# Performance work log

Measured on AMD Instinct MI355X. Metric: run time of the kernel, lower is better.

## Reference

```python
import jax, jax.numpy as jnp
import numpy as np

D_MODEL, D_BLOOM, N_HEADS = 768, 64, 4
HEAD_DIM = D_MODEL // N_HEADS


def setup_inputs() -> dict:
    key = jax.random.key(0)
    ks = jax.random.split(key, 16)
    B, S = 8, 1024
    s = 0.02
    return {
        "dnabert_hidden": jax.random.normal(ks[0], (B, S, D_MODEL), jnp.float32),
        "bloom_encoding": jax.random.uniform(ks[1], (B, S, D_BLOOM), jnp.float32),
        "Wq": jax.random.normal(ks[2], (D_MODEL, D_MODEL), jnp.float32) * s,
        "bq": jnp.zeros((D_MODEL,), jnp.float32),
        "Wk": jax.random.normal(ks[3], (D_BLOOM, D_MODEL), jnp.float32) * s,
        "bk": jnp.zeros((D_MODEL,), jnp.float32),
        "Wv": jax.random.normal(ks[4], (D_MODEL, D_MODEL), jnp.float32) * s,
        "bv": jnp.zeros((D_MODEL,), jnp.float32),
        "Wb1": jax.random.normal(ks[5], (D_BLOOM, N_HEADS * 2), jnp.float32) * s,
        "bb1": jnp.zeros((N_HEADS * 2,), jnp.float32),
        "Wb2": jax.random.normal(ks[6], (N_HEADS * 2, N_HEADS), jnp.float32) * s,
        "bb2": jnp.zeros((N_HEADS,), jnp.float32),
        "Wo": jax.random.normal(ks[7], (D_MODEL, D_MODEL), jnp.float32) * s,
        "bo": jnp.zeros((D_MODEL,), jnp.float32),
        "ln_g": jnp.ones((D_MODEL,), jnp.float32),
        "ln_b": jnp.zeros((D_MODEL,), jnp.float32),
    }


def reference(dnabert_hidden, bloom_encoding, Wq, bq, Wk, bk, Wv, bv,
              Wb1, bb1, Wb2, bb2, Wo, bo, ln_g, ln_b):
    B, S, _ = dnabert_hidden.shape
    H, Dh = N_HEADS, HEAD_DIM
    # projections -> [B, H, S, Dh]
    Q = (dnabert_hidden @ Wq + bq).reshape(B, S, H, Dh).transpose(0, 2, 1, 3)
    K = (bloom_encoding @ Wk + bk).reshape(B, S, H, Dh).transpose(0, 2, 1, 3)
    V = (dnabert_hidden @ Wv + bv).reshape(B, S, H, Dh).transpose(0, 2, 1, 3)
    scores = jnp.einsum('bhqd,bhkd->bhqk', Q, K) / jnp.sqrt(jnp.float32(Dh))
    # bloom bias MLP: [B, S, H] -> broadcast over query positions as [B, H, 1, S]
    h = jax.nn.gelu(bloom_encoding @ Wb1 + bb1, approximate=False)
    bias = (h @ Wb2 + bb2).transpose(0, 2, 1)[:, :, None, :]
    attn = jax.nn.softmax(scores + bias, axis=-1)  # dropout is identity in eval
    ctx = jnp.einsum('bhqk,bhkd->bhqd', attn, V)
    ctx = ctx.transpose(0, 2, 1, 3).reshape(B, S, H * Dh)
    out = ctx @ Wo + bo
    x = out + dnabert_hidden
    mu = jnp.mean(x, axis=-1, keepdims=True)
    var = jnp.var(x, axis=-1, keepdims=True)
    y = (x - mu) * jax.lax.rsqrt(var + 1e-5) * ln_g + ln_b
    return y, attn
```

## Files before the change

kernel.cpp:

```cpp
#include <hip/hip_runtime.h>
#include <hip/hip_bf16.h>
#include <math.h>
#include <stdint.h>

typedef __bf16 bf16;
typedef __bf16 bf16x8 __attribute__((ext_vector_type(8)));
typedef __bf16 bf16x4v __attribute__((ext_vector_type(4)));
typedef float f32x4 __attribute__((ext_vector_type(4)));

#define NHEADS 4
#define DM 768
#define DB 64
#define HD 192
#define BATCH 8
#define SEQ 1024
#define MROWS 8192
#define SCALE 0.07216878364870323f

__device__ __forceinline__ void gld_lds16(const void* g, void* l) {
  __builtin_amdgcn_global_load_lds(
      (__attribute__((address_space(1))) void*)(void*)g,
      (__attribute__((address_space(3))) void*)l, 16, 0, 0);
}

__global__ __launch_bounds__(256) void prologue(
    const float* __restrict__ Xd, bf16* __restrict__ Xd_bf,
    const float* __restrict__ Xb, bf16* __restrict__ Xb_bf,
    const float* __restrict__ Wq, const float* __restrict__ Wv,
    const float* __restrict__ Wk, const float* __restrict__ Wo,
    bf16* __restrict__ WT0, bf16* __restrict__ WT1,
    bf16* __restrict__ WT2, bf16* __restrict__ WT3,
    const float* __restrict__ Wb1, const float* __restrict__ bb1,
    const float* __restrict__ Wb2, const float* __restrict__ bb2,
    float* __restrict__ biasarr) {
  __shared__ float Lt[64 * 65];
  const int id = blockIdx.x;
  const int tid = threadIdx.x;
  if (id < 6656) {
    const float* in = (id < 6144) ? Xd : Xb;
    bf16* out = (id < 6144) ? Xd_bf : Xb_bf;
    long i = (long)(id < 6144 ? id : id - 6144) * 256 + tid;
    f32x4 v = *(const f32x4*)&in[i * 4];
    bf16x4v t;
    t[0] = (bf16)v[0]; t[1] = (bf16)v[1]; t[2] = (bf16)v[2]; t[3] = (bf16)v[3];
    *(bf16x4v*)&out[i * 4] = t;
  } else if (id < 6688) {
    int idx = (id - 6656) * 256 + tid;
    const float* x = Xb + (long)idx * DB;
    float h[8];
#pragma unroll
    for (int j = 0; j < 8; ++j) h[j] = bb1[j];
    for (int k = 0; k < DB; ++k) {
      float xv = x[k];
#pragma unroll
      for (int j = 0; j < 8; ++j) h[j] = fmaf(xv, Wb1[k * 8 + j], h[j]);
    }
#pragma unroll
    for (int j = 0; j < 8; ++j) {
      float a = h[j];
      h[j] = 0.5f * a * (1.0f + erff(a * 0.7071067811865476f));
    }
    int b = idx >> 10, s = idx & 1023;
#pragma unroll
    for (int o = 0; o < 4; ++o) {
      float a = bb2[o];
#pragma unroll
      for (int j = 0; j < 8; ++j) a = fmaf(h[j], Wb2[j * 4 + o], a);
      biasarr[((long)(b * 4 + o) << 10) + s] = a;
    }
  } else {
    int wi = id - 6688;
    const float* W;
    bf16* WT;
    int K, tIdx;
    if (wi < 144)      { W = Wq; WT = WT0; K = DM; tIdx = wi; }
    else if (wi < 288) { W = Wv; WT = WT1; K = DM; tIdx = wi - 144; }
    else if (wi < 300) { W = Wk; WT = WT2; K = DB; tIdx = wi - 288; }
    else               { W = Wo; WT = WT3; K = DM; tIdx = wi - 300; }
    const int tk0 = (tIdx / 12) * 64;
    const int tn0 = (tIdx % 12) * 64;
#pragma unroll
    for (int p = 0; p < 4; ++p) {
      int r = p * 16 + (tid >> 4);
      int c = (tid & 15) * 4;
      f32x4 v = *(const f32x4*)&W[(long)(tk0 + r) * DM + tn0 + c];
      Lt[r * 65 + c] = v[0]; Lt[r * 65 + c + 1] = v[1];
      Lt[r * 65 + c + 2] = v[2]; Lt[r * 65 + c + 3] = v[3];
    }
    __syncthreads();
    const int n = tid >> 2, kg = (tid & 3) * 16;
    bf16x8 o0, o1;
#pragma unroll
    for (int e = 0; e < 8; ++e) {
      o0[e] = (bf16)Lt[(kg + e) * 65 + n];
      o1[e] = (bf16)Lt[(kg + 8 + e) * 65 + n];
    }
    *(bf16x8*)&WT[(long)(tn0 + n) * K + tk0 + kg] = o0;
    *(bf16x8*)&WT[(long)(tn0 + n) * K + tk0 + kg + 8] = o1;
  }
}

__global__ __launch_bounds__(256) void rowsum_scale_f32(float* __restrict__ attn) {
  const int row = blockIdx.x * 4 + (threadIdx.x >> 6);
  const int lane = threadIdx.x & 63;
  float* ar = attn + ((long)row << 10);
  f32x4 v[4];
#pragma unroll
  for (int i = 0; i < 4; ++i) v[i] = *(const f32x4*)&ar[i * 256 + lane * 4];
  float s = 0.0f;
#pragma unroll
  for (int i = 0; i < 4; ++i)
#pragma unroll
    for (int j = 0; j < 4; ++j) s += v[i][j];
  for (int d = 1; d < 64; d <<= 1) s += __shfl_xor(s, d);
  float iv = 1.0f / s;
#pragma unroll
  for (int i = 0; i < 4; ++i) {
#pragma unroll
    for (int j = 0; j < 4; ++j) v[i][j] *= iv;
    *(f32x4*)&ar[i * 256 + lane * 4] = v[i];
  }
}

template <int MODE>
__global__ __launch_bounds__(256) void gemm_bt(
    const bf16* __restrict__ A, int lda,
    const bf16* __restrict__ BT, int ldb,
    const float* __restrict__ Af,
    int M, int N, int Kd,
    const float* __restrict__ cb1,
    const float* __restrict__ cb2,
    const float* __restrict__ resid,
    void* __restrict__ out, void* __restrict__ out2) {
  __shared__ __attribute__((aligned(16))) bf16 aL[2 * 128 * 32];
  __shared__ __attribute__((aligned(16))) bf16 bL[2 * 128 * 32];
  __shared__ float ivL[128];
  const int tid = threadIdx.x;
  const int lane = tid & 63;
  const int wid = tid >> 6;
  const int wr = wid >> 1, wc = wid & 1;
  int bx, by, bz;
  if constexpr (MODE == 2 || MODE == 7) {
    int idd = blockIdx.x;
    bz = idd & 31;
    int t = idd >> 5;
    bx = t & 7;
    by = t >> 3;
  } else if constexpr (MODE == 5 || MODE == 8) {
    int idd = blockIdx.x;
    bz = idd & 31;
    bx = (idd >> 5) & 1;
    by = idd >> 6;
  } else {
    bx = blockIdx.x; by = blockIdx.y; bz = 0;
  }
  const int m0 = by * 128, n0 = bx * 128;

  const bf16* Ab = A;
  const bf16* Bb = BT;
  const float* Afb = Af;
  if constexpr (MODE == 2 || MODE == 7) {
    long o = ((long)((bz >> 2) * SEQ)) * DM + (long)(bz & 3) * HD;
    Ab = A + o;
    Bb = BT + o;
  }
  if constexpr (MODE == 8) {
    Ab = A + ((long)bz << 20);
    Bb = BT + (((long)((bz >> 2) * DM + (bz & 3) * HD)) << 10);
  }
  if constexpr (MODE == 5) {
    Bb = BT + (((long)((bz >> 2) * DM + (bz & 3) * HD)) << 10);
    Afb = Af + ((long)bz << 20);
  }

  float iv0 = 0.f, iv1 = 0.f;
  if constexpr (MODE == 8) {
    if (tid < 128) {
      const float* p = cb2 + ((((long)bz << 10) + m0 + tid) << 4);
      float s = 0.0f;
#pragma unroll
      for (int i = 0; i < 16; ++i) s += p[i];
      ivL[tid] = 1.0f / s;
    }
    __syncthreads();
    iv0 = ivL[tid >> 2];
    iv1 = ivL[64 + (tid >> 2)];
  }

  f32x4 acc[4][4] = {};

  for (int k0 = 0; k0 < Kd; k0 += 64) {
#pragma unroll
    for (int h = 0; h < 2; ++h) {
      if constexpr (MODE == 5) {
#pragma unroll
        for (int p = 0; p < 2; ++p) {
          int f = (p * 256 + tid) * 8;
          int row = f >> 5, col = f & 31;
          const float* g = Afb + (long)(m0 + row) * lda + k0 + h * 32 + col;
          f32x4 x0 = *(const f32x4*)g;
          f32x4 x1 = *(const f32x4*)(g + 4);
          bf16x8 t;
          t[0] = (bf16)x0[0]; t[1] = (bf16)x0[1]; t[2] = (bf16)x0[2]; t[3] = (bf16)x0[3];
          t[4] = (bf16)x1[0]; t[5] = (bf16)x1[1]; t[6] = (bf16)x1[2]; t[7] = (bf16)x1[3];
          *(bf16x8*)&aL[h * 4096 + f] = t;
        }
      } else {
#pragma unroll
        for (int p = 0; p < 2; ++p) {
          int f = (p * 256 + tid) * 8;
          int row = f >> 5, col = f & 31;
          gld_lds16(Ab + (long)(m0 + row) * lda + k0 + h * 32 + col, &aL[h * 4096 + f]);
        }
      }
#pragma unroll
      for (int p = 0; p < 2; ++p) {
        int f = (p * 256 + tid) * 8;
        int row = f >> 5, col = f & 31;
        int nn = n0 + row;
        nn = nn < N ? nn : N - 1;
        gld_lds16(Bb + (long)nn * ldb + k0 + h * 32 + col, &bL[h * 4096 + f]);
      }
    }
    __syncthreads();

    if constexpr (MODE == 8) {
      if ((k0 < 512) == (bx == 0)) {
#pragma unroll
        for (int h = 0; h < 2; ++h)
#pragma unroll
          for (int p = 0; p < 2; ++p) {
            int f = (p * 256 + tid) * 8;
            int row = f >> 5, col = f & 31;
            bf16x8 e = *(const bf16x8*)&aL[h * 4096 + f];
            float iv = p ? iv1 : iv0;
            f32x4 w0, w1;
            w0[0] = (float)e[0] * iv; w0[1] = (float)e[1] * iv;
            w0[2] = (float)e[2] * iv; w0[3] = (float)e[3] * iv;
            w1[0] = (float)e[4] * iv; w1[1] = (float)e[5] * iv;
            w1[2] = (float)e[6] * iv; w1[3] = (float)e[7] * iv;
            float* ap = (float*)out2 + ((long)bz << 20) + ((long)(m0 + row) << 10)
                        + k0 + h * 32 + col;
            __builtin_nontemporal_store(w0, (f32x4*)ap);
            __builtin_nontemporal_store(w1, (f32x4*)(ap + 4));
          }
      }
    }

    const int rsel = lane & 15, ksel = (lane >> 4) * 8;
#pragma unroll
    for (int h = 0; h < 2; ++h) {
      bf16x8 af[4], bfr[4];
#pragma unroll
      for (int m = 0; m < 4; ++m)
        af[m] = *(const bf16x8*)&aL[h * 4096 + (wr * 64 + m * 16 + rsel) * 32 + ksel];
#pragma unroll
      for (int n = 0; n < 4; ++n)
        bfr[n] = *(const bf16x8*)&bL[h * 4096 + (wc * 64 + n * 16 + rsel) * 32 + ksel];
#pragma unroll
      for (int m = 0; m < 4; ++m)
#pragma unroll
        for (int n = 0; n < 4; ++n)
          acc[m][n] = __builtin_amdgcn_mfma_f32_16x16x32_bf16(af[m], bfr[n], acc[m][n], 0, 0, 0);
    }
    __syncthreads();
  }

  const int rl = (lane >> 4) * 4, cl = lane & 15;

  if constexpr (MODE == 2) {
    float bvv[4];
#pragma unroll
    for (int n = 0; n < 4; ++n)
      bvv[n] = cb2[(bz << 10) + n0 + wc * 64 + n * 16 + cl];
#pragma unroll
    for (int m = 0; m < 4; ++m)
#pragma unroll
      for (int n = 0; n < 4; ++n)
#pragma unroll
        for (int j = 0; j < 4; ++j)
          acc[m][n][j] = __expf(fmaf(acc[m][n][j], SCALE, bvv[n]));
    float* part = (float*)out2;
#pragma unroll
    for (int m = 0; m < 4; ++m) {
#pragma unroll
      for (int j = 0; j < 4; ++j) {
        float s = acc[m][0][j] + acc[m][1][j] + acc[m][2][j] + acc[m][3][j];
#pragma unroll
        for (int d = 1; d < 16; d <<= 1) s += __shfl_xor(s, d);
        if (cl == 0) {
          int mg = m0 + wr * 64 + m * 16 + rl + j;
          part[((((long)bz << 10) + mg) << 4) + bx * 2 + wc] = s;
        }
      }
    }
#pragma unroll
    for (int m = 0; m < 4; ++m)
#pragma unroll
      for (int n = 0; n < 4; ++n)
#pragma unroll
        for (int j = 0; j < 4; ++j) {
          int row = wr * 64 + m * 16 + rl + j;
          int col = wc * 64 + n * 16 + cl;
          bf16* Lt = (row < 64) ? &aL[row * 128 + col] : &bL[(row - 64) * 128 + col];
          *Lt = (bf16)acc[m][n][j];
        }
    __syncthreads();
#pragma unroll
    for (int it = 0; it < 8; ++it) {
      int row = it * 16 + (tid >> 4);
      int col = (tid & 15) * 8;
      bf16x8 v = (row < 64) ? *(const bf16x8*)&aL[row * 128 + col]
                            : *(const bf16x8*)&bL[(row - 64) * 128 + col];
      *(bf16x8*)&((bf16*)out)[((long)bz << 20) + ((long)(m0 + row) << 10) + n0 + col] = v;
    }
    return;
  }

  if constexpr (MODE == 6) {
    if (n0 >= DM) {
      const int d0 = n0 - DM;
      float bvv[4];
#pragma unroll
      for (int n = 0; n < 4; ++n)
        bvv[n] = cb2[d0 + wc * 64 + n * 16 + cl];
#pragma unroll
      for (int m = 0; m < 4; ++m)
#pragma unroll
        for (int n = 0; n < 4; ++n)
#pragma unroll
          for (int j = 0; j < 4; ++j) {
            int row = wr * 64 + m * 16 + rl + j;
            int col = wc * 64 + n * 16 + cl;
            int sw = row ^ ((col & 7) << 4);
            bf16 val = (bf16)(acc[m][n][j] + bvv[n]);
            if (col < 64) aL[col * 128 + sw] = val;
            else          bL[(col - 64) * 128 + sw] = val;
          }
      __syncthreads();
      const int b = m0 >> 10, s0 = m0 & 1023;
#pragma unroll
      for (int it = 0; it < 8; ++it) {
        int d = it * 16 + (tid >> 4);
        int s = (tid & 15) * 8;
        int sw = s ^ ((d & 7) << 4);
        bf16x8 v = (d < 64) ? *(const bf16x8*)&aL[d * 128 + sw]
                            : *(const bf16x8*)&bL[(d - 64) * 128 + sw];
        *(bf16x8*)&((bf16*)out2)[((long)(b * DM + d0 + d) << 10) + s0 + s] = v;
      }
      return;
    }
  }

  if constexpr (MODE == 0 || MODE == 6) {
    float bvv[4];
#pragma unroll
    for (int n = 0; n < 4; ++n)
      bvv[n] = cb1[n0 + wc * 64 + n * 16 + cl];
#pragma unroll
    for (int m = 0; m < 4; ++m)
#pragma unroll
      for (int n = 0; n < 4; ++n)
#pragma unroll
        for (int j = 0; j < 4; ++j) {
          int row = wr * 64 + m * 16 + rl + j;
          int col = wc * 64 + n * 16 + cl;
          bf16 val = (bf16)(acc[m][n][j] + bvv[n]);
          if (row < 64) aL[row * 128 + col] = val;
          else          bL[(row - 64) * 128 + col] = val;
        }
    __syncthreads();
#pragma unroll
    for (int it = 0; it < 8; ++it) {
      int row = it * 16 + (tid >> 4);
      int col = (tid & 15) * 8;
      bf16x8 v = (row < 64) ? *(const bf16x8*)&aL[row * 128 + col]
                            : *(const bf16x8*)&bL[(row - 64) * 128 + col];
      *(bf16x8*)&((bf16*)out)[(long)(m0 + row) * DM + n0 + col] = v;
    }
    return;
  }

  if constexpr (MODE == 8) {
#pragma unroll
    for (int m = 0; m < 4; ++m)
#pragma unroll
      for (int n = 0; n < 4; ++n)
#pragma unroll
        for (int j = 0; j < 4; ++j) {
          int row = wr * 64 + m * 16 + rl + j;
          int col = wc * 64 + n * 16 + cl;
          bf16 val = (bf16)(acc[m][n][j] * ivL[row]);
          if (row < 64) aL[row * 128 + col] = val;
          else          bL[(row - 64) * 128 + col] = val;
        }
    __syncthreads();
    const int b = bz >> 2, h = bz & 3;
#pragma unroll
    for (int it = 0; it < 8; ++it) {
      int row = it * 16 + (tid >> 4);
      int col = (tid & 15) * 8;
      int ng = n0 + col;
      if (ng < HD) {
        bf16x8 v = (row < 64) ? *(const bf16x8*)&aL[row * 128 + col]
                              : *(const bf16x8*)&bL[(row - 64) * 128 + col];
        *(bf16x8*)&((bf16*)out)[(long)(b * SEQ + m0 + row) * DM + h * HD + ng] = v;
      }
    }
    return;
  }

#pragma unroll
  for (int m = 0; m < 4; ++m) {
#pragma unroll
    for (int n = 0; n < 4; ++n) {
      int ng = n0 + wc * 64 + n * 16 + cl;
      if (ng >= N) continue;
#pragma unroll
      for (int j = 0; j < 4; ++j) {
        int mg = m0 + wr * 64 + m * 16 + rl + j;
        float v = acc[m][n][j];
        if constexpr (MODE == 7) {
          ((float*)out)[((long)bz << 20) + ((long)mg << 10) + ng] =
              __expf(fmaf(v, SCALE, cb2[(bz << 10) + ng]));
        } else if constexpr (MODE == 5) {
          ((bf16*)out)[(long)((bz >> 2) * SEQ + mg) * DM + (bz & 3) * HD + ng] = (bf16)v;
        } else {
          long o = (long)mg * DM + ng;
          ((float*)out)[o] = v + cb1[ng] + resid[o];
        }
      }
    }
  }
}

__global__ __launch_bounds__(256) void layernorm_rows(float* x, const float* __restrict__ gam,
                                                      const float* __restrict__ bet) {
  int row = blockIdx.x * 4 + (threadIdx.x >> 6);
  int lane = threadIdx.x & 63;
  float* r = x + (long)row * DM;
  f32x4 v[3];
#pragma unroll
  for (int i = 0; i < 3; ++i) v[i] = *(const f32x4*)&r[i * 256 + lane * 4];
  float s = 0.0f, ss = 0.0f;
#pragma unroll
  for (int i = 0; i < 3; ++i)
#pragma unroll
    for (int j = 0; j < 4; ++j) {
      s += v[i][j];
      ss += v[i][j] * v[i][j];
    }
  for (int d = 1; d < 64; d <<= 1) {
    s += __shfl_xor(s, d);
    ss += __shfl_xor(ss, d);
  }
  float mu = s * (1.0f / 768.0f);
  float var = ss * (1.0f / 768.0f) - mu * mu;
  float rs = 1.0f / sqrtf(var + 1e-5f);
#pragma unroll
  for (int i = 0; i < 3; ++i) {
#pragma unroll
    for (int j = 0; j < 4; ++j) {
      int c = i * 256 + lane * 4 + j;
      v[i][j] = (v[i][j] - mu) * rs * gam[c] + bet[c];
    }
    *(f32x4*)&r[i * 256 + lane * 4] = v[i];
  }
}

extern "C" void kernel_launch(void* const* d_in, const int* in_sizes, int n_in,
                              void* d_out, int out_size, void* d_ws, size_t ws_size,
                              hipStream_t stream) {
  const float* Xd = (const float*)d_in[0];
  const float* Xb = (const float*)d_in[1];
  const float* Wq = (const float*)d_in[2];
  const float* bq = (const float*)d_in[3];
  const float* Wk = (const float*)d_in[4];
  const float* bk = (const float*)d_in[5];
  const float* Wv = (const float*)d_in[6];
  const float* bv = (const float*)d_in[7];
  const float* Wb1 = (const float*)d_in[8];
  const float* bb1 = (const float*)d_in[9];
  const float* Wb2 = (const float*)d_in[10];
  const float* bb2 = (const float*)d_in[11];
  const float* Wo = (const float*)d_in[12];
  const float* bo = (const float*)d_in[13];
  const float* lng = (const float*)d_in[14];
  const float* lnb = (const float*)d_in[15];

  float* y = (float*)d_out;
  float* attn = y + (long)MROWS * DM;

  char* w = (char*)d_ws;
  bf16* Xd_bf = (bf16*)w; w += (long)MROWS * DM * 2;
  bf16* Xb_bf = (bf16*)w; w += (long)MROWS * DB * 2;
  bf16* WqvT = (bf16*)w; w += (long)2 * DM * DM * 2;
  bf16* WkT = (bf16*)w; w += (long)DM * DB * 2;
  bf16* WoT = (bf16*)w; w += (long)DM * DM * 2;
  bf16* Qb = (bf16*)w; w += (long)MROWS * DM * 2;
  bf16* Kb = (bf16*)w; w += (long)MROWS * DM * 2;
  bf16* VTb = (bf16*)w; w += (long)MROWS * DM * 2;
  float* biasarr = (float*)w; w += (long)BATCH * NHEADS * SEQ * 4;
  float* part = (float*)w; w += (long)32 * SEQ * 16 * 4;
  bf16* Sb = (bf16*)w; w += (long)32 * SEQ * SEQ * 2;
  const bool useS = ((size_t)(w - (char*)d_ws)) <= ws_size;
  bf16* ctxb = Xd_bf;

  dim3 blk(256);
  prologue<<<7132, blk, 0, stream>>>(Xd, Xd_bf, Xb, Xb_bf, Wq, Wv, Wk, Wo,
                                     WqvT, WqvT + (long)DM * DM, WkT, WoT,
                                     Wb1, bb1, Wb2, bb2, biasarr);

  gemm_bt<0><<<dim3(6, 64, 1), blk, 0, stream>>>(Xb_bf, DB, WkT, DB, nullptr, MROWS, DM, DB,
                                                 bk, nullptr, nullptr, Kb, nullptr);
  gemm_bt<6><<<dim3(12, 64, 1), blk, 0, stream>>>(Xd_bf, DM, WqvT, DM, nullptr, MROWS, 2 * DM, DM,
                                                  bq, bv, nullptr, Qb, VTb);
  if (useS) {
    gemm_bt<2><<<2048, blk, 0, stream>>>(Qb, DM, Kb, DM, nullptr, SEQ, SEQ, HD,
                                         nullptr, biasarr, nullptr, Sb, part);
    gemm_bt<8><<<512, blk, 0, stream>>>(Sb, SEQ, VTb, SEQ, nullptr, SEQ, HD, SEQ,
                                        nullptr, part, nullptr, ctxb, attn);
  } else {
    gemm_bt<7><<<2048, blk, 0, stream>>>(Qb, DM, Kb, DM, nullptr, SEQ, SEQ, HD,
                                         nullptr, biasarr, nullptr, attn, nullptr);
    rowsum_scale_f32<<<8192, blk, 0, stream>>>(attn);
    gemm_bt<5><<<512, blk, 0, stream>>>(nullptr, SEQ, VTb, SEQ, attn, SEQ, HD, SEQ,
                                        nullptr, nullptr, nullptr, ctxb, nullptr);
  }
  gemm_bt<4><<<dim3(6, 64, 1), blk, 0, stream>>>(ctxb, DM, WoT, DM, nullptr, MROWS, DM, DM,
                                                 bo, nullptr, Xd, y, nullptr);
  layernorm_rows<<<2048, 256, 0, stream>>>(y, lng, lnb);
}
```

Baseline: 187.2 us.

## Replace PV gemm with dedicated 64x192 tile kernel covering full head dim

Adds a dedicated P·V kernel that gives each block 64 query rows and the full 192-wide head dimension. The old path used 128x128 tiles with two N-blocks, which wasted half of the second tile (192 padded to 256) and re-read the probability tile twice. Each block now writes its own normalized attn rows, so the k0-split write logic is gone. It also flattens the grids of the other GEMMs so that M-blocks are the fastest-varying index, which changes L2 reuse of the weight tiles.

```diff
diff --git a/kernel.cpp b/kernel.cpp
--- a/kernel.cpp
+++ b/kernel.cpp
@@ -122,6 +122,111 @@
   }
 }
 
+__global__ __launch_bounds__(256) void pv_attn(
+    const bf16* __restrict__ E, const bf16* __restrict__ VT,
+    const float* __restrict__ part, bf16* __restrict__ ctx,
+    float* __restrict__ attn) {
+  __shared__ __attribute__((aligned(16))) bf16 aL[2 * 64 * 32];
+  __shared__ __attribute__((aligned(16))) bf16 bL[2 * 192 * 32];
+  __shared__ float ivL[64];
+  const int tid = threadIdx.x;
+  const int lane = tid & 63;
+  const int wid = tid >> 6;
+  const int wr = wid >> 1, wc = wid & 1;
+  const int id = blockIdx.x;
+  const int bz = id & 31;
+  const int by = id >> 5;
+  const int m0 = by * 64;
+  const int b = bz >> 2, h = bz & 3;
+
+  const bf16* Ab = E + ((long)bz << 20);
+  const bf16* Bb = VT + (((long)(b * DM + h * HD)) << 10);
+
+  if (tid < 64) {
+    const float* p = part + ((((long)bz << 10) + m0 + tid) << 4);
+    float s = 0.0f;
+#pragma unroll
+    for (int i = 0; i < 16; ++i) s += p[i];
+    ivL[tid] = 1.0f / s;
+  }
+  __syncthreads();
+  const float iv0 = ivL[tid >> 2];
+
+  f32x4 acc[2][6] = {};
+  const int rsel = lane & 15, ksel = (lane >> 4) * 8;
+
+  for (int k0 = 0; k0 < SEQ; k0 += 64) {
+#pragma unroll
+    for (int h2 = 0; h2 < 2; ++h2) {
+      {
+        int f = tid * 8;
+        int row = f >> 5, col = f & 31;
+        gld_lds16(Ab + (long)(m0 + row) * SEQ + k0 + h2 * 32 + col, &aL[h2 * 2048 + f]);
+      }
+#pragma unroll
+      for (int p = 0; p < 3; ++p) {
+        int f = (p * 256 + tid) * 8;
+        int row = f >> 5, col = f & 31;
+        gld_lds16(Bb + (long)row * SEQ + k0 + h2 * 32 + col, &bL[h2 * 6144 + f]);
+      }
+    }
+    __syncthreads();
+
+#pragma unroll
+    for (int h2 = 0; h2 < 2; ++h2) {
+      int f = tid * 8;
+      int row = f >> 5, col = f & 31;
+      bf16x8 e = *(const bf16x8*)&aL[h2 * 2048 + f];
+      f32x4 w0, w1;
+      w0[0] = (float)e[0] * iv0; w0[1] = (float)e[1] * iv0;
+      w0[2] = (float)e[2] * iv0; w0[3] = (float)e[3] * iv0;
+      w1[0] = (float)e[4] * iv0; w1[1] = (float)e[5] * iv0;
+      w1[2] = (float)e[6] * iv0; w1[3] = (float)e[7] * iv0;
+      float* ap = attn + ((long)bz << 20) + ((long)(m0 + row) << 10) + k0 + h2 * 32 + col;
+      __builtin_nontemporal_store(w0, (f32x4*)ap);
+      __builtin_nontemporal_store(w1, (f32x4*)(ap + 4));
+    }
+
+#pragma unroll
+    for (int h2 = 0; h2 < 2; ++h2) {
+      bf16x8 af[2], bfr[6];
+#pragma unroll
+      for (int m = 0; m < 2; ++m)
+        af[m] = *(const bf16x8*)&aL[h2 * 2048 + (wr * 32 + m * 16 + rsel) * 32 + ksel];
+#pragma unroll
+      for (int n = 0; n < 6; ++n)
+        bfr[n] = *(const bf16x8*)&bL[h2 * 6144 + (wc * 96 + n * 16 + rsel) * 32 + ksel];
+#pragma unroll
+      for (int m = 0; m < 2; ++m)
+#pragma unroll
+        for (int n = 0; n < 6; ++n)
+          acc[m][n] = __builtin_amdgcn_mfma_f32_16x16x32_bf16(af[m], bfr[n], acc[m][n], 0, 0, 0);
+    }
+    __syncthreads();
+  }
+
+  const int rl = (lane >> 4) * 4, cl = lane & 15;
+#pragma unroll
+  for (int m = 0; m < 2; ++m)
+#pragma unroll
+    for (int n = 0; n < 6; ++n)
+#pragma unroll
+      for (int j = 0; j < 4; ++j) {
+        int row = wr * 32 + m * 16 + rl + j;
+        int col = wc * 96 + n * 16 + cl;
+        bL[row * 192 + col] = (bf16)(acc[m][n][j] * ivL[row]);
+      }
+  __syncthreads();
+#pragma unroll
+  for (int it = 0; it < 6; ++it) {
+    int idx2 = it * 256 + tid;
+    int row = idx2 / 24;
+    int col = (idx2 % 24) * 8;
+    bf16x8 v = *(const bf16x8*)&bL[row * 192 + col];
+    *(bf16x8*)&ctx[(long)(b * SEQ + m0 + row) * DM + h * HD + col] = v;
+  }
+}
+
 template <int MODE>
 __global__ __launch_bounds__(256) void gemm_bt(
     const bf16* __restrict__ A, int lda,
@@ -134,7 +239,6 @@
     void* __restrict__ out, void* __restrict__ out2) {
   __shared__ __attribute__((aligned(16))) bf16 aL[2 * 128 * 32];
   __shared__ __attribute__((aligned(16))) bf16 bL[2 * 128 * 32];
-  __shared__ float ivL[128];
   const int tid = threadIdx.x;
   const int lane = tid & 63;
   const int wid = tid >> 6;
@@ -146,13 +250,16 @@
     int t = idd >> 5;
     bx = t & 7;
     by = t >> 3;
-  } else if constexpr (MODE == 5 || MODE == 8) {
+  } else if constexpr (MODE == 5) {
     int idd = blockIdx.x;
     bz = idd & 31;
     bx = (idd >> 5) & 1;
     by = idd >> 6;
   } else {
-    bx = blockIdx.x; by = blockIdx.y; bz = 0;
+    int idd = blockIdx.x;
+    by = idd & 63;
+    bx = idd >> 6;
+    bz = 0;
   }
   const int m0 = by * 128, n0 = bx * 128;
 
@@ -164,27 +271,9 @@
     Ab = A + o;
     Bb = BT + o;
   }
-  if constexpr (MODE == 8) {
-    Ab = A + ((long)bz << 20);
-    Bb = BT + (((long)((bz >> 2) * DM + (bz & 3) * HD)) << 10);
-  }
   if constexpr (MODE == 5) {
     Bb = BT + (((long)((bz >> 2) * DM + (bz & 3) * HD)) << 10);
     Afb = Af + ((long)bz << 20);
-  }
-
-  float iv0 = 0.f, iv1 = 0.f;
-  if constexpr (MODE == 8) {
-    if (tid < 128) {
-      const float* p = cb2 + ((((long)bz << 10) + m0 + tid) << 4);
-      float s = 0.0f;
-#pragma unroll
-      for (int i = 0; i < 16; ++i) s += p[i];
-      ivL[tid] = 1.0f / s;
-    }
-    __syncthreads();
-    iv0 = ivL[tid >> 2];
-    iv1 = ivL[64 + (tid >> 2)];
   }
 
   f32x4 acc[4][4] = {};
@@ -224,29 +313,6 @@
     }
     __syncthreads();
 
-    if constexpr (MODE == 8) {
-      if ((k0 < 512) == (bx == 0)) {
-#pragma unroll
-        for (int h = 0; h < 2; ++h)
-#pragma unroll
-          for (int p = 0; p < 2; ++p) {
-            int f = (p * 256 + tid) * 8;
-            int row = f >> 5, col = f & 31;
-            bf16x8 e = *(const bf16x8*)&aL[h * 4096 + f];
-            float iv = p ? iv1 : iv0;
-            f32x4 w0, w1;
-            w0[0] = (float)e[0] * iv; w0[1] = (float)e[1] * iv;
-            w0[2] = (float)e[2] * iv; w0[3] = (float)e[3] * iv;
-            w1[0] = (float)e[4] * iv; w1[1] = (float)e[5] * iv;
-            w1[2] = (float)e[6] * iv; w1[3] = (float)e[7] * iv;
-            float* ap = (float*)out2 + ((long)bz << 20) + ((long)(m0 + row) << 10)
-                        + k0 + h * 32 + col;
-            __builtin_nontemporal_store(w0, (f32x4*)ap);
-            __builtin_nontemporal_store(w1, (f32x4*)(ap + 4));
-          }
-      }
-    }
-
     const int rsel = lane & 15, ksel = (lane >> 4) * 8;
 #pragma unroll
     for (int h = 0; h < 2; ++h) {
@@ -377,35 +443,6 @@
       bf16x8 v = (row < 64) ? *(const bf16x8*)&aL[row * 128 + col]
                             : *(const bf16x8*)&bL[(row - 64) * 128 + col];
       *(bf16x8*)&((bf16*)out)[(long)(m0 + row) * DM + n0 + col] = v;
-    }
-    return;
-  }
-
-  if constexpr (MODE == 8) {
-#pragma unroll
-    for (int m = 0; m < 4; ++m)
-#pragma unroll
-      for (int n = 0; n < 4; ++n)
-#pragma unroll
-        for (int j = 0; j < 4; ++j) {
-          int row = wr * 64 + m * 16 + rl + j;
-          int col = wc * 64 + n * 16 + cl;
-          bf16 val = (bf16)(acc[m][n][j] * ivL[row]);
-          if (row < 64) aL[row * 128 + col] = val;
-          else          bL[(row - 64) * 128 + col] = val;
-        }
-    __syncthreads();
-    const int b = bz >> 2, h = bz & 3;
-#pragma unroll
-    for (int it = 0; it < 8; ++it) {
-      int row = it * 16 + (tid >> 4);
-      int col = (tid & 15) * 8;
-      int ng = n0 + col;
-      if (ng < HD) {
-        bf16x8 v = (row < 64) ? *(const bf16x8*)&aL[row * 128 + col]
-                              : *(const bf16x8*)&bL[(row - 64) * 128 + col];
-        *(bf16x8*)&((bf16*)out)[(long)(b * SEQ + m0 + row) * DM + h * HD + ng] = v;
-      }
     }
     return;
   }
@@ -511,15 +548,14 @@
                                      WqvT, WqvT + (long)DM * DM, WkT, WoT,
                                      Wb1, bb1, Wb2, bb2, biasarr);
 
-  gemm_bt<0><<<dim3(6, 64, 1), blk, 0, stream>>>(Xb_bf, DB, WkT, DB, nullptr, MROWS, DM, DB,
-                                                 bk, nullptr, nullptr, Kb, nullptr);
-  gemm_bt<6><<<dim3(12, 64, 1), blk, 0, stream>>>(Xd_bf, DM, WqvT, DM, nullptr, MROWS, 2 * DM, DM,
-                                                  bq, bv, nullptr, Qb, VTb);
+  gemm_bt<0><<<384, blk, 0, stream>>>(Xb_bf, DB, WkT, DB, nullptr, MROWS, DM, DB,
+                                      bk, nullptr, nullptr, Kb, nullptr);
+  gemm_bt<6><<<768, blk, 0, stream>>>(Xd_bf, DM, WqvT, DM, nullptr, MROWS, 2 * DM, DM,
+                                      bq, bv, nullptr, Qb, VTb);
   if (useS) {
     gemm_bt<2><<<2048, blk, 0, stream>>>(Qb, DM, Kb, DM, nullptr, SEQ, SEQ, HD,
                                          nullptr, biasarr, nullptr, Sb, part);
-    gemm_bt<8><<<512, blk, 0, stream>>>(Sb, SEQ, VTb, SEQ, nullptr, SEQ, HD, SEQ,
-                                        nullptr, part, nullptr, ctxb, attn);
+    pv_attn<<<512, blk, 0, stream>>>(Sb, VTb, part, ctxb, attn);
   } else {
     gemm_bt<7><<<2048, blk, 0, stream>>>(Qb, DM, Kb, DM, nullptr, SEQ, SEQ, HD,
                                          nullptr, biasarr, nullptr, attn, nullptr);
@@ -527,7 +563,7 @@
     gemm_bt<5><<<512, blk, 0, stream>>>(nullptr, SEQ, VTb, SEQ, attn, SEQ, HD, SEQ,
                                         nullptr, nullptr, nullptr, ctxb, nullptr);
   }
-  gemm_bt<4><<<dim3(6, 64, 1), blk, 0, stream>>>(ctxb, DM, WoT, DM, nullptr, MROWS, DM, DM,
-                                                 bo, nullptr, Xd, y, nullptr);
+  gemm_bt<4><<<384, blk, 0, stream>>>(ctxb, DM, WoT, DM, nullptr, MROWS, DM, DM,
+                                      bo, nullptr, Xd, y, nullptr);
   layernorm_rows<<<2048, 256, 0, stream>>>(y, lng, lnb);
 }
```

Measured after the change: 175.7 us. 6.1% less time.
